# Kernel tuning notes

Hardware: AMD Instinct MI355X
Metric: run time of the kernel (lower is better)

## Reference

```python
import jax, jax.numpy as jnp
import numpy as np
import math

IN_FEATURE = 4096
OUT_FEATURE = 11008

def setup_inputs() -> dict:
    key = jax.random.key(0)
    k1, k2 = jax.random.split(key)
    x = jax.random.normal(k1, (4, 2048, IN_FEATURE), dtype=jnp.float32)
    # int8 weights in [-128, 127]; keep as int8 (stored as int32 spec-wise but cast to int8 here)
    int8_weights = jax.random.randint(k2, (OUT_FEATURE, IN_FEATURE), -128, 128, dtype=jnp.int32).astype(jnp.int8)
    scaler = jnp.float32(1.0 / 128.0 / math.sqrt(IN_FEATURE))
    return {"x": x, "int8_weights": int8_weights, "scaler": scaler}

def reference(x, int8_weights, scaler):
    # Dequantize int8 weights to fp32, then dense matmul: y = x @ W^T
    fp_weights = int8_weights.astype(jnp.float32) * scaler  # [O, I]
    return jnp.einsum('bsi,oi->bso', x, fp_weights)
```

## Files before the change

### kernel.cpp

```cpp
#include <hip/hip_runtime.h>

typedef __attribute__((ext_vector_type(8))) short short8;
typedef __attribute__((ext_vector_type(8))) unsigned short ushort8;
typedef __attribute__((ext_vector_type(4))) float f32x4;
typedef __attribute__((ext_vector_type(4))) float float4v;
typedef __attribute__((ext_vector_type(4))) int int4v;

#define GLB_CAST(p) ((const __attribute__((address_space(1))) void*)(p))
#define LDS_CAST(p) ((__attribute__((address_space(3))) void*)(p))

__device__ __forceinline__ unsigned short f2bf_rne(float f) {
  unsigned u = __builtin_bit_cast(unsigned, f);
  u += 0x7fffu + ((u >> 16) & 1u);
  return (unsigned short)(u >> 16);
}

__device__ __forceinline__ bool w_looks_int32(const int* wi) {
  bool all_small = true;
#pragma unroll
  for (int i = 0; i < 16; ++i) {
    int v = wi[i];
    if (v > 127 || v < -128) all_small = false;
  }
  return all_small;
}


__global__ void init_slot_kernel(unsigned* slot) { *slot = 0u; }

__global__ void absmax_kernel(const float4v* __restrict__ x, unsigned* __restrict__ slot, long n4) {
  float m = 0.f;
  long stride = (long)gridDim.x * blockDim.x;
  for (long i = blockIdx.x * (long)blockDim.x + threadIdx.x; i < n4; i += stride) {
    float4v v = x[i];
#pragma unroll
    for (int j = 0; j < 4; ++j) m = fmaxf(m, fabsf(v[j]));
  }
#pragma unroll
  for (int off = 32; off >= 1; off >>= 1) m = fmaxf(m, __shfl_down(m, off));
  if ((threadIdx.x & 63) == 0) atomicMax(slot, __float_as_uint(m));
}

__global__ void quant_x_kernel(const float* __restrict__ x, int4v* __restrict__ q,
                               const unsigned* __restrict__ slot, long n16) {
  const float k = 127.f / __uint_as_float(*slot);
  long stride = (long)gridDim.x * blockDim.x;
  for (long i = blockIdx.x * (long)blockDim.x + threadIdx.x; i < n16; i += stride) {
    const float4v* xp = (const float4v*)(x + i * 16);
    int4v r;
#pragma unroll
    for (int qd = 0; qd < 4; ++qd) {
      float4v v = xp[qd];
      int w = 0;
#pragma unroll
      for (int j = 0; j < 4; ++j) {
        int b = (int)__builtin_rintf(fminf(fmaxf(v[j] * k, -127.f), 127.f));
        w |= (b & 0xff) << (8 * j);
      }
      r[qd] = w;
    }
    q[i] = r;
  }
}

__global__ void pack_w_kernel(const void* __restrict__ w, int4v* __restrict__ wq, long n16) {
  const bool is32 = w_looks_int32((const int*)w);
  long stride = (long)gridDim.x * blockDim.x;
  for (long i = blockIdx.x * (long)blockDim.x + threadIdx.x; i < n16; i += stride) {
    int4v r;
    if (is32) {
      const int4v* w4 = (const int4v*)w;
#pragma unroll
      for (int qd = 0; qd < 4; ++qd) {
        int4v raw = w4[i * 4 + qd];
        r[qd] = (raw[0] & 0xff) | ((raw[1] & 0xff) << 8) | ((raw[2] & 0xff) << 16) | (raw[3] << 24);
      }
    } else {
      r = reinterpret_cast<const int4v*>(w)[i];
    }
    wq[i] = r;
  }
}

__global__ __launch_bounds__(512, 2) void gemm256_i8_kernel(
    const signed char* __restrict__ A, const signed char* __restrict__ Bw,
    float* __restrict__ C, const unsigned* __restrict__ slot,
    const float* __restrict__ scaler, int M, int N, int K) {
  __shared__ __align__(16) char lds[131072];

  const int tid  = threadIdx.x;
  const int lane = tid & 63;
  const int wv   = tid >> 6;
  const int wm   = wv >> 2;
  const int wn   = wv & 3;
  const int fr   = lane & 15;
  const int fq   = lane >> 4;

  const int nwg  = gridDim.x;
  const int orig = blockIdx.x;
  const int ntn  = N >> 8;
  const int ntm  = M >> 8;
  int tm, tn;
  if (((nwg & 7) == 0) && ((ntm & 7) == 0)) {
    const int c     = orig & 7;
    const int w     = orig >> 3;
    const int bandh = ntm >> 3;
    tm = c * bandh + (w % bandh);
    tn = w / bandh;
  } else {
    tm = orig / ntn;
    tn = orig - tm * ntn;
  }
  const long rowBase = (long)tm << 8;
  const long colBase = (long)tn << 8;

  const int    srow  = tid >> 3;
  const int    scolb = (((tid & 7) ^ (srow & 7)) << 4);
  const size_t rowb  = (size_t)K;
  const size_t hstep = rowb << 7;
  const size_t r64   = rowb << 6;
  const char*  gA    = (const char*)A + (rowBase + srow) * rowb + scolb;
  const char*  gB    = (const char*)Bw + (colBase + srow) * rowb + scolb;
  const int    dst   = tid << 4;

#define STAGE(gsrc, loff)                                                                              \
  do {                                                                                                 \
    __builtin_amdgcn_global_load_lds(GLB_CAST(gsrc), LDS_CAST(lds + (loff) + dst), 16, 0, 0);          \
    __builtin_amdgcn_global_load_lds(GLB_CAST((gsrc) + r64), LDS_CAST(lds + (loff) + 8192 + dst), 16, 0, 0); \
  } while (0)

  int offA[4][2], offB[2][2];
#pragma unroll
  for (int i = 0; i < 4; ++i) {
    const int lr = i * 32 + wm * 16 + fr;
    const int sw = (lr & 7) << 4;
#pragma unroll
    for (int kk = 0; kk < 2; ++kk) offA[i][kk] = lr * 128 + ((kk * 64 + fq * 16) ^ sw);
  }
#pragma unroll
  for (int j = 0; j < 2; ++j) {
    const int lr = j * 64 + wn * 16 + fr;
    const int sw = (lr & 7) << 4;
#pragma unroll
    for (int kk = 0; kk < 2; ++kk) offB[j][kk] = lr * 128 + ((kk * 64 + fq * 16) ^ sw);
  }

  int4v acc[8][4] = {};
  int4v af[4][2], bf[4][2];
  const int nt = K >> 7;

  STAGE(gA,         0);
  STAGE(gB,         32768);
  STAGE(gA + hstep, 16384);
  STAGE(gB + hstep, 49152);
  asm volatile("s_waitcnt vmcnt(4)" ::: "memory");
  if (nt > 1) {
    STAGE(gA + 128,         65536);
    STAGE(gB + 128,         65536 + 32768);
    STAGE(gA + hstep + 128, 65536 + 16384);
  }
  asm volatile("s_waitcnt vmcnt(6)" ::: "memory");
  __builtin_amdgcn_s_barrier();

  for (int t = 0; t < nt; ++t) {
    const int cur = (t & 1) << 16;
    const int nxt = cur ^ 65536;
    const size_t kof1 = (size_t)(t + 1) << 7;
    const size_t kof2 = (size_t)(t + 2) << 7;

#pragma unroll
    for (int i = 0; i < 4; ++i) {
      af[i][0] = *(const int4v*)(lds + cur + offA[i][0]);
      af[i][1] = *(const int4v*)(lds + cur + offA[i][1]);
    }
#pragma unroll
    for (int j = 0; j < 2; ++j) {
      bf[j][0] = *(const int4v*)(lds + cur + 32768 + offB[j][0]);
      bf[j][1] = *(const int4v*)(lds + cur + 32768 + offB[j][1]);
    }
    if (t + 1 < nt) STAGE(gB + hstep + kof1, nxt + 49152);
    __builtin_amdgcn_s_barrier();
    asm volatile("s_waitcnt lgkmcnt(0)");
    __builtin_amdgcn_s_setprio(1);
#pragma unroll
    for (int i = 0; i < 4; ++i)
#pragma unroll
      for (int j = 0; j < 2; ++j) {
        acc[i][j] = __builtin_amdgcn_mfma_i32_16x16x64_i8(af[i][0], bf[j][0], acc[i][j], 0, 0, 0);
        acc[i][j] = __builtin_amdgcn_mfma_i32_16x16x64_i8(af[i][1], bf[j][1], acc[i][j], 0, 0, 0);
      }
    __builtin_amdgcn_s_setprio(0);
    __builtin_amdgcn_s_barrier();

#pragma unroll
    for (int j = 2; j < 4; ++j) {
      bf[j][0] = *(const int4v*)(lds + cur + 49152 + offB[j - 2][0]);
      bf[j][1] = *(const int4v*)(lds + cur + 49152 + offB[j - 2][1]);
    }
    if (t + 2 < nt) STAGE(gA + kof2, cur + 0);
    __builtin_amdgcn_s_barrier();
    asm volatile("s_waitcnt lgkmcnt(0)");
    __builtin_amdgcn_s_setprio(1);
#pragma unroll
    for (int i = 0; i < 4; ++i)
#pragma unroll
      for (int j = 2; j < 4; ++j) {
        acc[i][j] = __builtin_amdgcn_mfma_i32_16x16x64_i8(af[i][0], bf[j][0], acc[i][j], 0, 0, 0);
        acc[i][j] = __builtin_amdgcn_mfma_i32_16x16x64_i8(af[i][1], bf[j][1], acc[i][j], 0, 0, 0);
      }
    __builtin_amdgcn_s_setprio(0);
    __builtin_amdgcn_s_barrier();

#pragma unroll
    for (int i = 0; i < 4; ++i) {
      af[i][0] = *(const int4v*)(lds + cur + 16384 + offA[i][0]);
      af[i][1] = *(const int4v*)(lds + cur + 16384 + offA[i][1]);
    }
    if (t + 2 < nt) STAGE(gB + kof2, cur + 32768);
    __builtin_amdgcn_s_barrier();
    asm volatile("s_waitcnt lgkmcnt(0)");
    __builtin_amdgcn_s_setprio(1);
#pragma unroll
    for (int i = 0; i < 4; ++i)
#pragma unroll
      for (int j = 2; j < 4; ++j) {
        acc[4 + i][j] = __builtin_amdgcn_mfma_i32_16x16x64_i8(af[i][0], bf[j][0], acc[4 + i][j], 0, 0, 0);
        acc[4 + i][j] = __builtin_amdgcn_mfma_i32_16x16x64_i8(af[i][1], bf[j][1], acc[4 + i][j], 0, 0, 0);
      }
    __builtin_amdgcn_s_setprio(0);
    __builtin_amdgcn_s_barrier();

    if (t + 2 < nt) STAGE(gA + hstep + kof2, cur + 16384);
    __builtin_amdgcn_s_barrier();
    __builtin_amdgcn_s_setprio(1);
#pragma unroll
    for (int i = 0; i < 4; ++i)
#pragma unroll
      for (int j = 0; j < 2; ++j) {
        acc[4 + i][j] = __builtin_amdgcn_mfma_i32_16x16x64_i8(af[i][0], bf[j][0], acc[4 + i][j], 0, 0, 0);
        acc[4 + i][j] = __builtin_amdgcn_mfma_i32_16x16x64_i8(af[i][1], bf[j][1], acc[4 + i][j], 0, 0, 0);
      }
    __builtin_amdgcn_s_setprio(0);
    if (t + 2 < nt)      { asm volatile("s_waitcnt vmcnt(6)" ::: "memory"); }
    else if (t + 1 < nt) { asm volatile("s_waitcnt vmcnt(0)" ::: "memory"); }
    if (t + 1 < nt) __builtin_amdgcn_s_barrier();
  }
#undef STAGE

  const float sc = __uint_as_float(*slot) * (*scaler) * (1.f / 127.f);
#pragma unroll
  for (int mi = 0; mi < 8; ++mi) {
#pragma unroll
    for (int j = 0; j < 4; ++j) {
      const long row = rowBase + mi * 32 + wm * 16 + fq * 4 + j;
      float* cp = C + row * (long)N + colBase + wn * 16 + fr;
#pragma unroll
      for (int nj = 0; nj < 4; ++nj) cp[(size_t)nj * 64] = (float)acc[mi][nj][j] * sc;
    }
  }
}


__global__ void cvt_x_kernel(const float* __restrict__ x, ushort8* __restrict__ xh, long n8) {
  long stride = (long)gridDim.x * blockDim.x;
  for (long i = blockIdx.x * (long)blockDim.x + threadIdx.x; i < n8; i += stride) {
    float4v a = reinterpret_cast<const float4v*>(x)[2 * i + 0];
    float4v b = reinterpret_cast<const float4v*>(x)[2 * i + 1];
    ushort8 r;
#pragma unroll
    for (int j = 0; j < 4; ++j) {
      r[j]     = f2bf_rne(a[j]);
      r[4 + j] = f2bf_rne(b[j]);
    }
    xh[i] = r;
  }
}

__global__ void cvt_w_kernel(const void* __restrict__ w, ushort8* __restrict__ wh,
                             const float* __restrict__ sp, long n16) {
  const float s = *sp;
  const bool is32 = w_looks_int32((const int*)w);
  long stride = (long)gridDim.x * blockDim.x;
  for (long i = blockIdx.x * (long)blockDim.x + threadIdx.x; i < n16; i += stride) {
    unsigned short tmp[16];
    if (is32) {
      const int4v* w4 = (const int4v*)w;
#pragma unroll
      for (int q = 0; q < 4; ++q) {
        int4v raw = w4[i * 4 + q];
#pragma unroll
        for (int j = 0; j < 4; ++j) tmp[4 * q + j] = f2bf_rne((float)raw[j] * s);
      }
    } else {
      int4v raw = reinterpret_cast<const int4v*>(w)[i];
#pragma unroll
      for (int q = 0; q < 4; ++q) {
        int v = raw[q];
        tmp[4 * q + 0] = f2bf_rne((float)(int)(signed char)(v & 0xff) * s);
        tmp[4 * q + 1] = f2bf_rne((float)(int)(signed char)((v >> 8) & 0xff) * s);
        tmp[4 * q + 2] = f2bf_rne((float)(int)(signed char)((v >> 16) & 0xff) * s);
        tmp[4 * q + 3] = f2bf_rne((float)(v >> 24) * s);
      }
    }
    ushort8 r0, r1;
#pragma unroll
    for (int j = 0; j < 8; ++j) { r0[j] = tmp[j]; r1[j] = tmp[8 + j]; }
    wh[2 * i + 0] = r0;
    wh[2 * i + 1] = r1;
  }
}

#define BM 128
#define BN 128
#define BK 32
__global__ __launch_bounds__(256) void gemm_bt_kernel(
    const unsigned short* __restrict__ A, const unsigned short* __restrict__ Bw,
    float* __restrict__ C, int M, int N, int K) {
  __shared__ __align__(16) unsigned short As[BM * BK];
  __shared__ __align__(16) unsigned short Bs[BN * BK];
  const int t = threadIdx.x, lane = t & 63, wv = t >> 6, wr = wv >> 1, wc = wv & 1;
  const long rowBase = (long)blockIdx.y * BM, colBase = (long)blockIdx.x * BN;
  const int r0 = t >> 2, cb0 = (t & 3) * 16, r1 = r0 + 64;
  const char* gA0 = (const char*)(A + (rowBase + r0) * (long)K) + cb0;
  const char* gA1 = (const char*)(A + (rowBase + r1) * (long)K) + cb0;
  const char* gB0 = (const char*)(Bw + (colBase + r0) * (long)K) + cb0;
  const char* gB1 = (const char*)(Bw + (colBase + r1) * (long)K) + cb0;
  char* lA0 = (char*)As + wv * 1024; char* lA1 = (char*)As + 4096 + wv * 1024;
  char* lB0 = (char*)Bs + wv * 1024; char* lB1 = (char*)Bs + 4096 + wv * 1024;
  const int fr = lane & 15, kb = (lane >> 4) * 16;
  const char* aBase = (const char*)As + (wr * 64 + fr) * (BK * 2) + kb;
  const char* bBase = (const char*)Bs + (wc * 64 + fr) * (BK * 2) + kb;
  f32x4 acc[4][4] = {};
  for (int k0 = 0; k0 < K; k0 += BK) {
    const long koff = (long)k0 * 2;
    __builtin_amdgcn_global_load_lds(GLB_CAST(gA0 + koff), LDS_CAST(lA0), 16, 0, 0);
    __builtin_amdgcn_global_load_lds(GLB_CAST(gA1 + koff), LDS_CAST(lA1), 16, 0, 0);
    __builtin_amdgcn_global_load_lds(GLB_CAST(gB0 + koff), LDS_CAST(lB0), 16, 0, 0);
    __builtin_amdgcn_global_load_lds(GLB_CAST(gB1 + koff), LDS_CAST(lB1), 16, 0, 0);
    __syncthreads();
    short8 af[4], bfv[4];
#pragma unroll
    for (int mi = 0; mi < 4; ++mi) af[mi] = *reinterpret_cast<const short8*>(aBase + mi * 16 * (BK * 2));
#pragma unroll
    for (int nj = 0; nj < 4; ++nj) bfv[nj] = *reinterpret_cast<const short8*>(bBase + nj * 16 * (BK * 2));
#pragma unroll
    for (int mi = 0; mi < 4; ++mi)
#pragma unroll
      for (int nj = 0; nj < 4; ++nj)
        acc[mi][nj] = __builtin_amdgcn_mfma_f32_16x16x32_bf16(af[mi], bfv[nj], acc[mi][nj], 0, 0, 0);
    __syncthreads();
  }
  const int fq = lane >> 4;
#pragma unroll
  for (int mi = 0; mi < 4; ++mi)
#pragma unroll
    for (int j = 0; j < 4; ++j) {
      const long row = rowBase + wr * 64 + mi * 16 + fq * 4 + j;
      float* cp = C + row * (long)N + colBase + wc * 64 + fr;
#pragma unroll
      for (int nj = 0; nj < 4; ++nj) cp[nj * 16] = acc[mi][nj][j];
    }
}

__global__ void gemm_naive_kernel(const float* __restrict__ x, const void* __restrict__ w,
                                  const float* __restrict__ sp, float* __restrict__ out,
                                  int M, int N, int K) {
  const bool is32 = w_looks_int32((const int*)w);
  int n = blockIdx.x * 16 + threadIdx.x;
  int m = blockIdx.y * 16 + threadIdx.y;
  if (m >= M || n >= N) return;
  const float* xr = x + (long)m * K;
  float acc = 0.f;
  if (is32) {
    const int* wr_ = (const int*)w + (long)n * K;
    for (int k = 0; k < K; ++k) acc += xr[k] * (float)wr_[k];
  } else {
    const signed char* wr_ = (const signed char*)w + (long)n * K;
    for (int k = 0; k < K; ++k) acc += xr[k] * (float)wr_[k];
  }
  out[(long)m * N + n] = acc * (*sp);
}

extern "C" void kernel_launch(void* const* d_in, const int* in_sizes, int n_in,
                              void* d_out, int out_size, void* d_ws, size_t ws_size,
                              hipStream_t stream) {
  const float* x      = (const float*)d_in[0];
  const void*  w      = (const void*)d_in[1];
  const float* scaler = (const float*)d_in[2];
  float*       out    = (float*)d_out;

  const int K = 4096;
  const int N = 11008;
  const int M = in_sizes[0] / K;

  const size_t xq_bytes = (size_t)M * K;
  const size_t wq_bytes = (size_t)N * K;
  const size_t i8_need  = xq_bytes + wq_bytes + 64;

  if ((M % 256 == 0) && (N % 256 == 0) && (K % 128 == 0) && ws_size >= i8_need) {
    signed char* xq   = (signed char*)d_ws;
    signed char* wq   = (signed char*)((char*)d_ws + xq_bytes);
    unsigned*    slot = (unsigned*)((char*)d_ws + xq_bytes + wq_bytes);

    init_slot_kernel<<<1, 1, 0, stream>>>(slot);
    absmax_kernel<<<1024, 256, 0, stream>>>((const float4v*)x, slot, (long)M * K / 4);
    quant_x_kernel<<<2048, 256, 0, stream>>>(x, (int4v*)xq, slot, (long)M * K / 16);
    pack_w_kernel<<<2048, 256, 0, stream>>>(w, (int4v*)wq, (long)N * K / 16);
    gemm256_i8_kernel<<<dim3((M / 256) * (N / 256)), 512, 0, stream>>>(
        xq, wq, out, slot, scaler, M, N, K);
    return;
  }

  const size_t xh_bytes = (size_t)M * K * 2;
  const size_t wh_bytes = (size_t)N * K * 2;
  if (ws_size < xh_bytes + wh_bytes) {
    dim3 g((N + 15) / 16, (M + 15) / 16), b(16, 16);
    gemm_naive_kernel<<<g, b, 0, stream>>>(x, w, scaler, out, M, N, K);
    return;
  }

  unsigned short* xh = (unsigned short*)d_ws;
  unsigned short* wh = (unsigned short*)((char*)d_ws + xh_bytes);
  cvt_x_kernel<<<2048, 256, 0, stream>>>(x, (ushort8*)xh, (long)M * K / 8);
  cvt_w_kernel<<<2048, 256, 0, stream>>>(w, (ushort8*)wh, scaler, (long)N * K / 16);
  gemm_bt_kernel<<<dim3(N / BN, M / BM), 256, 0, stream>>>(xh, wh, out, M, N, K);
}
```

Measured before the change: 531.2 us.

## Switch int8 GEMM to 32x32x32 MFMA, skip weight copy when already int8

The inner GEMM now uses 32x32x32 int8 MFMA tiles instead of 16x16x64, which changes per-wave fragment layout, LDS offsets and the epilogue store mapping. The weight packing kernel now also clears the absmax slot, which removes the separate init launch. It returns early when the weights are already int8, and the GEMM then reads the raw weights directly instead of a copied buffer, avoiding one full pass over the weight matrix. Larger MFMA tiles reduce LDS fragment reads per MAC but change register pressure and the store pattern.

After: 594.2 us. 1.12x slower.

```diff
diff --git a/kernel.cpp b/kernel.cpp
--- a/kernel.cpp
+++ b/kernel.cpp
@@ -5,6 +5,7 @@
 typedef __attribute__((ext_vector_type(4))) float f32x4;
 typedef __attribute__((ext_vector_type(4))) float float4v;
 typedef __attribute__((ext_vector_type(4))) int int4v;
+typedef __attribute__((ext_vector_type(16))) int int16v;
 
 #define GLB_CAST(p) ((const __attribute__((address_space(1))) void*)(p))
 #define LDS_CAST(p) ((__attribute__((address_space(3))) void*)(p))
@@ -26,7 +27,23 @@
 }
 
 
-__global__ void init_slot_kernel(unsigned* slot) { *slot = 0u; }
+__global__ void pack_w_kernel(const void* __restrict__ w, int4v* __restrict__ wq,
+                              unsigned* __restrict__ slot, long n16) {
+  if (blockIdx.x == 0 && threadIdx.x == 0) *slot = 0u;
+  const bool is32 = w_looks_int32((const int*)w);
+  if (!is32) return;
+  long stride = (long)gridDim.x * blockDim.x;
+  for (long i = blockIdx.x * (long)blockDim.x + threadIdx.x; i < n16; i += stride) {
+    const int4v* w4 = (const int4v*)w;
+    int4v r;
+#pragma unroll
+    for (int qd = 0; qd < 4; ++qd) {
+      int4v raw = w4[i * 4 + qd];
+      r[qd] = (raw[0] & 0xff) | ((raw[1] & 0xff) << 8) | ((raw[2] & 0xff) << 16) | (raw[3] << 24);
+    }
+    wq[i] = r;
+  }
+}
 
 __global__ void absmax_kernel(const float4v* __restrict__ x, unsigned* __restrict__ slot, long n4) {
   float m = 0.f;
@@ -63,38 +80,22 @@
   }
 }
 
-__global__ void pack_w_kernel(const void* __restrict__ w, int4v* __restrict__ wq, long n16) {
-  const bool is32 = w_looks_int32((const int*)w);
-  long stride = (long)gridDim.x * blockDim.x;
-  for (long i = blockIdx.x * (long)blockDim.x + threadIdx.x; i < n16; i += stride) {
-    int4v r;
-    if (is32) {
-      const int4v* w4 = (const int4v*)w;
-#pragma unroll
-      for (int qd = 0; qd < 4; ++qd) {
-        int4v raw = w4[i * 4 + qd];
-        r[qd] = (raw[0] & 0xff) | ((raw[1] & 0xff) << 8) | ((raw[2] & 0xff) << 16) | (raw[3] << 24);
-      }
-    } else {
-      r = reinterpret_cast<const int4v*>(w)[i];
-    }
-    wq[i] = r;
-  }
-}
-
-__global__ __launch_bounds__(512, 2) void gemm256_i8_kernel(
-    const signed char* __restrict__ A, const signed char* __restrict__ Bw,
-    float* __restrict__ C, const unsigned* __restrict__ slot,
-    const float* __restrict__ scaler, int M, int N, int K) {
+__global__ __launch_bounds__(512, 2) void gemm256_i8x32_kernel(
+    const signed char* __restrict__ wraw, const signed char* __restrict__ wq,
+    const signed char* __restrict__ A, float* __restrict__ C,
+    const unsigned* __restrict__ slot, const float* __restrict__ scaler,
+    int M, int N, int K) {
   __shared__ __align__(16) char lds[131072];
+
+  const signed char* Bw = w_looks_int32((const int*)wraw) ? wq : wraw;
 
   const int tid  = threadIdx.x;
   const int lane = tid & 63;
   const int wv   = tid >> 6;
   const int wm   = wv >> 2;
   const int wn   = wv & 3;
-  const int fr   = lane & 15;
-  const int fq   = lane >> 4;
+  const int r31  = lane & 31;
+  const int hi   = lane >> 5;
 
   const int nwg  = gridDim.x;
   const int orig = blockIdx.x;
@@ -129,24 +130,23 @@
     __builtin_amdgcn_global_load_lds(GLB_CAST((gsrc) + r64), LDS_CAST(lds + (loff) + 8192 + dst), 16, 0, 0); \
   } while (0)
 
-  int offA[4][2], offB[2][2];
-#pragma unroll
-  for (int i = 0; i < 4; ++i) {
-    const int lr = i * 32 + wm * 16 + fr;
+  int offA[2][4], offB[4];
+#pragma unroll
+  for (int m01 = 0; m01 < 2; ++m01) {
+    const int lr = wm * 64 + m01 * 32 + r31;
     const int sw = (lr & 7) << 4;
 #pragma unroll
-    for (int kk = 0; kk < 2; ++kk) offA[i][kk] = lr * 128 + ((kk * 64 + fq * 16) ^ sw);
-  }
-#pragma unroll
-  for (int j = 0; j < 2; ++j) {
-    const int lr = j * 64 + wn * 16 + fr;
+    for (int kk = 0; kk < 4; ++kk) offA[m01][kk] = lr * 128 + ((kk * 32 + hi * 16) ^ sw);
+  }
+  {
+    const int lr = wn * 32 + r31;
     const int sw = (lr & 7) << 4;
 #pragma unroll
-    for (int kk = 0; kk < 2; ++kk) offB[j][kk] = lr * 128 + ((kk * 64 + fq * 16) ^ sw);
-  }
-
-  int4v acc[8][4] = {};
-  int4v af[4][2], bf[4][2];
+    for (int kk = 0; kk < 4; ++kk) offB[kk] = lr * 128 + ((kk * 32 + hi * 16) ^ sw);
+  }
+
+  int16v acc[4][2] = {};
+  int4v af[2][4], bf0[4], bf1[4];
   const int nt = K >> 7;
 
   STAGE(gA,         0);
@@ -169,64 +169,50 @@
     const size_t kof2 = (size_t)(t + 2) << 7;
 
 #pragma unroll
-    for (int i = 0; i < 4; ++i) {
-      af[i][0] = *(const int4v*)(lds + cur + offA[i][0]);
-      af[i][1] = *(const int4v*)(lds + cur + offA[i][1]);
-    }
-#pragma unroll
-    for (int j = 0; j < 2; ++j) {
-      bf[j][0] = *(const int4v*)(lds + cur + 32768 + offB[j][0]);
-      bf[j][1] = *(const int4v*)(lds + cur + 32768 + offB[j][1]);
-    }
+    for (int m01 = 0; m01 < 2; ++m01)
+#pragma unroll
+      for (int kk = 0; kk < 4; ++kk) af[m01][kk] = *(const int4v*)(lds + cur + offA[m01][kk]);
+#pragma unroll
+    for (int kk = 0; kk < 4; ++kk) bf0[kk] = *(const int4v*)(lds + cur + 32768 + offB[kk]);
     if (t + 1 < nt) STAGE(gB + hstep + kof1, nxt + 49152);
     __builtin_amdgcn_s_barrier();
     asm volatile("s_waitcnt lgkmcnt(0)");
     __builtin_amdgcn_s_setprio(1);
 #pragma unroll
-    for (int i = 0; i < 4; ++i)
-#pragma unroll
-      for (int j = 0; j < 2; ++j) {
-        acc[i][j] = __builtin_amdgcn_mfma_i32_16x16x64_i8(af[i][0], bf[j][0], acc[i][j], 0, 0, 0);
-        acc[i][j] = __builtin_amdgcn_mfma_i32_16x16x64_i8(af[i][1], bf[j][1], acc[i][j], 0, 0, 0);
-      }
+    for (int m01 = 0; m01 < 2; ++m01)
+#pragma unroll
+      for (int kk = 0; kk < 4; ++kk)
+        acc[m01][0] = __builtin_amdgcn_mfma_i32_32x32x32_i8(af[m01][kk], bf0[kk], acc[m01][0], 0, 0, 0);
     __builtin_amdgcn_s_setprio(0);
     __builtin_amdgcn_s_barrier();
 
 #pragma unroll
-    for (int j = 2; j < 4; ++j) {
-      bf[j][0] = *(const int4v*)(lds + cur + 49152 + offB[j - 2][0]);
-      bf[j][1] = *(const int4v*)(lds + cur + 49152 + offB[j - 2][1]);
-    }
+    for (int kk = 0; kk < 4; ++kk) bf1[kk] = *(const int4v*)(lds + cur + 49152 + offB[kk]);
     if (t + 2 < nt) STAGE(gA + kof2, cur + 0);
     __builtin_amdgcn_s_barrier();
     asm volatile("s_waitcnt lgkmcnt(0)");
     __builtin_amdgcn_s_setprio(1);
 #pragma unroll
-    for (int i = 0; i < 4; ++i)
-#pragma unroll
-      for (int j = 2; j < 4; ++j) {
-        acc[i][j] = __builtin_amdgcn_mfma_i32_16x16x64_i8(af[i][0], bf[j][0], acc[i][j], 0, 0, 0);
-        acc[i][j] = __builtin_amdgcn_mfma_i32_16x16x64_i8(af[i][1], bf[j][1], acc[i][j], 0, 0, 0);
-      }
+    for (int m01 = 0; m01 < 2; ++m01)
+#pragma unroll
+      for (int kk = 0; kk < 4; ++kk)
+        acc[m01][1] = __builtin_amdgcn_mfma_i32_32x32x32_i8(af[m01][kk], bf1[kk], acc[m01][1], 0, 0, 0);
     __builtin_amdgcn_s_setprio(0);
     __builtin_amdgcn_s_barrier();
 
 #pragma unroll
-    for (int i = 0; i < 4; ++i) {
-      af[i][0] = *(const int4v*)(lds + cur + 16384 + offA[i][0]);
-      af[i][1] = *(const int4v*)(lds + cur + 16384 + offA[i][1]);
-    }
+    for (int m01 = 0; m01 < 2; ++m01)
+#pragma unroll
+      for (int kk = 0; kk < 4; ++kk) af[m01][kk] = *(const int4v*)(lds + cur + 16384 + offA[m01][kk]);
     if (t + 2 < nt) STAGE(gB + kof2, cur + 32768);
     __builtin_amdgcn_s_barrier();
     asm volatile("s_waitcnt lgkmcnt(0)");
     __builtin_amdgcn_s_setprio(1);
 #pragma unroll
-    for (int i = 0; i < 4; ++i)
-#pragma unroll
-      for (int j = 2; j < 4; ++j) {
-        acc[4 + i][j] = __builtin_amdgcn_mfma_i32_16x16x64_i8(af[i][0], bf[j][0], acc[4 + i][j], 0, 0, 0);
-        acc[4 + i][j] = __builtin_amdgcn_mfma_i32_16x16x64_i8(af[i][1], bf[j][1], acc[4 + i][j], 0, 0, 0);
-      }
+    for (int m01 = 0; m01 < 2; ++m01)
+#pragma unroll
+      for (int kk = 0; kk < 4; ++kk)
+        acc[2 + m01][1] = __builtin_amdgcn_mfma_i32_32x32x32_i8(af[m01][kk], bf1[kk], acc[2 + m01][1], 0, 0, 0);
     __builtin_amdgcn_s_setprio(0);
     __builtin_amdgcn_s_barrier();
 
@@ -234,12 +220,10 @@
     __builtin_amdgcn_s_barrier();
     __builtin_amdgcn_s_setprio(1);
 #pragma unroll
-    for (int i = 0; i < 4; ++i)
-#pragma unroll
-      for (int j = 0; j < 2; ++j) {
-        acc[4 + i][j] = __builtin_amdgcn_mfma_i32_16x16x64_i8(af[i][0], bf[j][0], acc[4 + i][j], 0, 0, 0);
-        acc[4 + i][j] = __builtin_amdgcn_mfma_i32_16x16x64_i8(af[i][1], bf[j][1], acc[4 + i][j], 0, 0, 0);
-      }
+    for (int m01 = 0; m01 < 2; ++m01)
+#pragma unroll
+      for (int kk = 0; kk < 4; ++kk)
+        acc[2 + m01][0] = __builtin_amdgcn_mfma_i32_32x32x32_i8(af[m01][kk], bf0[kk], acc[2 + m01][0], 0, 0, 0);
     __builtin_amdgcn_s_setprio(0);
     if (t + 2 < nt)      { asm volatile("s_waitcnt vmcnt(6)" ::: "memory"); }
     else if (t + 1 < nt) { asm volatile("s_waitcnt vmcnt(0)" ::: "memory"); }
@@ -249,13 +233,15 @@
 
   const float sc = __uint_as_float(*slot) * (*scaler) * (1.f / 127.f);
 #pragma unroll
-  for (int mi = 0; mi < 8; ++mi) {
-#pragma unroll
-    for (int j = 0; j < 4; ++j) {
-      const long row = rowBase + mi * 32 + wm * 16 + fq * 4 + j;
-      float* cp = C + row * (long)N + colBase + wn * 16 + fr;
-#pragma unroll
-      for (int nj = 0; nj < 4; ++nj) cp[(size_t)nj * 64] = (float)acc[mi][nj][j] * sc;
+  for (int mb = 0; mb < 4; ++mb) {
+#pragma unroll
+    for (int nb = 0; nb < 2; ++nb) {
+#pragma unroll
+      for (int r = 0; r < 16; ++r) {
+        const long row = rowBase + (mb >> 1) * 128 + wm * 64 + (mb & 1) * 32 +
+                         (r & 3) + 8 * (r >> 2) + 4 * hi;
+        C[row * (long)N + colBase + nb * 128 + wn * 32 + r31] = (float)acc[mb][nb][r] * sc;
+      }
     }
   }
 }
@@ -402,12 +388,11 @@
     signed char* wq   = (signed char*)((char*)d_ws + xq_bytes);
     unsigned*    slot = (unsigned*)((char*)d_ws + xq_bytes + wq_bytes);
 
-    init_slot_kernel<<<1, 1, 0, stream>>>(slot);
+    pack_w_kernel<<<2048, 256, 0, stream>>>(w, (int4v*)wq, slot, (long)N * K / 16);
     absmax_kernel<<<1024, 256, 0, stream>>>((const float4v*)x, slot, (long)M * K / 4);
     quant_x_kernel<<<2048, 256, 0, stream>>>(x, (int4v*)xq, slot, (long)M * K / 16);
-    pack_w_kernel<<<2048, 256, 0, stream>>>(w, (int4v*)wq, (long)N * K / 16);
-    gemm256_i8_kernel<<<dim3((M / 256) * (N / 256)), 512, 0, stream>>>(
-        xq, wq, out, slot, scaler, M, N, K);
+    gemm256_i8x32_kernel<<<dim3((M / 256) * (N / 256)), 512, 0, stream>>>(
+        (const signed char*)w, wq, xq, out, slot, scaler, M, N, K);
     return;
   }
 
```
